# Kernel tuning notes

Hardware: AMD Instinct MI355X
Metric: run time of the kernel (lower is better)

The kernel has to match this reference:

```python
import jax, jax.numpy as jnp
import numpy as np

B, N, E = 8, 1024, 256
IN_DIMS, D_MODEL, H = 2, 64, 4
DH = D_MODEL // H  # 16


def _linear_params(key, fan_in, fan_out):
    k1, k2 = jax.random.split(key)
    bound = 1.0 / np.sqrt(fan_in)
    W = jax.random.uniform(k1, (fan_in, fan_out), jnp.float32, -bound, bound)
    b = jax.random.uniform(k2, (fan_out,), jnp.float32, -bound, bound)
    return W, b


def setup_inputs() -> dict:
    key = jax.random.key(0)
    ks = jax.random.split(key, 12)
    x = jax.random.normal(ks[0], (B, N, IN_DIMS), jnp.float32)
    edge_inital = jax.random.normal(ks[1], (B, H, E, DH), jnp.float32)
    C_edge_inital = jax.random.normal(ks[2], (B, H, E, DH), jnp.float32)
    G = jax.random.uniform(ks[3], (B, E, N), jnp.float32)
    C_G = jax.random.uniform(ks[4], (B, E, N), jnp.float32)
    W_emb, b_emb = _linear_params(ks[5], IN_DIMS, D_MODEL)
    W_q, b_q = _linear_params(ks[6], D_MODEL, D_MODEL)
    W_k, b_k = _linear_params(ks[7], D_MODEL, D_MODEL)
    W_eq, b_eq = _linear_params(ks[8], DH, DH)
    W_ek, b_ek = _linear_params(ks[9], DH, DH)
    W_ceq, b_ceq = _linear_params(ks[10], DH, DH)
    W_cek, b_cek = _linear_params(ks[11], DH, DH)
    return dict(x=x, edge_inital=edge_inital, C_edge_inital=C_edge_inital, G=G, C_G=C_G,
                W_emb=W_emb, b_emb=b_emb, W_q=W_q, b_q=b_q, W_k=W_k, b_k=b_k,
                W_eq=W_eq, b_eq=b_eq, W_ek=W_ek, b_ek=b_ek,
                W_ceq=W_ceq, b_ceq=b_ceq, W_cek=W_cek, b_cek=b_cek)


def _split_heads(t):
    # [B, N, D_MODEL] -> [B, H, N, DH]
    b, n, _ = t.shape
    return t.reshape(b, n, H, DH).transpose(0, 2, 1, 3)


def _branch(q, k, edge, Gm, We_q, be_q, We_k, be_k, scale):
    eq = edge @ We_q + be_q          # [B,H,E,DH]
    ek = edge @ We_k + be_k
    div = Gm.sum(axis=1)[:, None, :, None]  # [B,1,N,1]
    gq = q + jnp.einsum('ben,bhec->bhnc', Gm, eq) / div
    gk = k + jnp.einsum('ben,bhec->bhnc', Gm, ek) / div
    scores = jnp.einsum('bhnc,bhmc->bhnm', gq, gk) / scale
    return jax.nn.softmax(scores, axis=-1)


def reference(x, edge_inital, C_edge_inital, G, C_G,
              W_emb, b_emb, W_q, b_q, W_k, b_k,
              W_eq, b_eq, W_ek, b_ek, W_ceq, b_ceq, W_cek, b_cek):
    scale = jnp.sqrt(jnp.float32(D_MODEL))
    emb = x @ W_emb + b_emb                 # [B,N,D]
    q = _split_heads(emb @ W_q + b_q)       # [B,H,N,DH]
    k = _split_heads(emb @ W_k + b_k)
    g_att = _branch(q, k, edge_inital, G, W_eq, b_eq, W_ek, b_ek, scale)
    cg_att = _branch(q, k, C_edge_inital, C_G, W_ceq, b_ceq, W_cek, b_cek, scale)
    return (g_att, cg_att)
```

## Files before the change

### kernel.cpp

```cpp
#include <hip/hip_runtime.h>
#include <math.h>

#define BB     8
#define NN     1024
#define EE     256
#define DMODEL 64
#define HH     4
#define DHH    16

#define WS_Q    0
#define WS_K    524288
#define WS_EQ   1048576
#define WS_GQ   1572864
#define WS_GKT  2621440

__global__ __launch_bounds__(256) void qk_kernel(
    const float* __restrict__ x, const float* __restrict__ W_emb,
    const float* __restrict__ b_emb, const float* __restrict__ W_q,
    const float* __restrict__ b_q, const float* __restrict__ W_k,
    const float* __restrict__ b_k, float* __restrict__ ws) {
  __shared__ float semb[4][DMODEL];
  const int tid = threadIdx.x;
  const int p = tid >> 6, d = tid & 63;
  const int pos = blockIdx.x * 4 + p;
  const float x0 = x[pos * 2 + 0];
  const float x1 = x[pos * 2 + 1];
  semb[p][d] = fmaf(x0, W_emb[d], fmaf(x1, W_emb[DMODEL + d], b_emb[d]));
  __syncthreads();
  float accq = b_q[d], acck = b_k[d];
#pragma unroll 8
  for (int e = 0; e < DMODEL; ++e) {
    const float ev = semb[p][e];
    accq = fmaf(ev, W_q[e * DMODEL + d], accq);
    acck = fmaf(ev, W_k[e * DMODEL + d], acck);
  }
  const int b = pos >> 10, n = pos & (NN - 1);
  const int h = d >> 4, c = d & 15;
  const int oidx = ((b * HH + h) * NN + n) * DHH + c;
  ws[WS_Q + oidx] = accq;
  ws[WS_K + oidx] = acck;
}

__global__ __launch_bounds__(256) void edge_proj_kernel(
    const float* __restrict__ edge, const float* __restrict__ C_edge,
    const float* __restrict__ W_eq, const float* __restrict__ b_eq,
    const float* __restrict__ W_ek, const float* __restrict__ b_ek,
    const float* __restrict__ W_ceq, const float* __restrict__ b_ceq,
    const float* __restrict__ W_cek, const float* __restrict__ b_cek,
    float* __restrict__ ws) {
  const int t = blockIdx.x >> 5;
  const int row = ((blockIdx.x & 31) << 8) + threadIdx.x;
  const float* __restrict__ src = (t < 2) ? edge : C_edge;
  const float* __restrict__ W =
      (t == 0) ? W_eq : (t == 1) ? W_ek : (t == 2) ? W_ceq : W_cek;
  const float* __restrict__ bias =
      (t == 0) ? b_eq : (t == 1) ? b_ek : (t == 2) ? b_ceq : b_cek;
  float in[16];
  const float4* s4 = (const float4*)(src + row * 16);
#pragma unroll
  for (int i = 0; i < 4; ++i) {
    const float4 v = s4[i];
    in[4 * i + 0] = v.x; in[4 * i + 1] = v.y;
    in[4 * i + 2] = v.z; in[4 * i + 3] = v.w;
  }
  float outv[16];
#pragma unroll
  for (int c = 0; c < 16; ++c) outv[c] = bias[c];
#pragma unroll
  for (int cp = 0; cp < 16; ++cp) {
    const float iv = in[cp];
#pragma unroll
    for (int c = 0; c < 16; ++c) outv[c] = fmaf(iv, W[cp * 16 + c], outv[c]);
  }
  float4* o4 = (float4*)(ws + WS_EQ + t * 131072 + row * 16);
#pragma unroll
  for (int i = 0; i < 4; ++i)
    o4[i] = make_float4(outv[4 * i + 0], outv[4 * i + 1], outv[4 * i + 2],
                        outv[4 * i + 3]);
}

__global__ __launch_bounds__(256) void gqgk_kernel(
    const float* __restrict__ G, const float* __restrict__ C_G,
    float* __restrict__ ws) {
  const int sub = blockIdx.x & 7;
  const int mat = blockIdx.x >> 3;
  const int h = mat & 3;
  const int b = (mat >> 2) & 7;
  const int br = mat >> 5;
  const int nchunk = sub >> 1;
  const int c0 = (sub & 1) * 8;
  const int n = (nchunk << 8) + threadIdx.x;
  const float* __restrict__ Gm = br ? C_G : G;
  const float* __restrict__ eqp =
      ws + WS_EQ + (br * 2 + 0) * 131072 + (b * HH + h) * EE * 16 + c0;
  const float* __restrict__ ekp =
      ws + WS_EQ + (br * 2 + 1) * 131072 + (b * HH + h) * EE * 16 + c0;
  const float* __restrict__ gcol = Gm + b * EE * NN + n;
  float accq[8] = {0.f, 0.f, 0.f, 0.f, 0.f, 0.f, 0.f, 0.f};
  float acck[8] = {0.f, 0.f, 0.f, 0.f, 0.f, 0.f, 0.f, 0.f};
  float div = 0.f;
#pragma unroll 4
  for (int e = 0; e < EE; ++e) {
    const float g = gcol[e * NN];
    div += g;
#pragma unroll
    for (int c = 0; c < 8; ++c) {
      accq[c] = fmaf(g, eqp[e * 16 + c], accq[c]);
      acck[c] = fmaf(g, ekp[e * 16 + c], acck[c]);
    }
  }
  const float inv = 1.0f / div;
  const int qidx = ((b * HH + h) * NN + n) * 16 + c0;
  const float* __restrict__ qrow = ws + WS_Q + qidx;
  const float* __restrict__ krow = ws + WS_K + qidx;
  float* __restrict__ gq = ws + WS_GQ + (mat * NN + n) * 16 + c0;
  float* __restrict__ gkT = ws + WS_GKT + mat * 16 * NN + n;
#pragma unroll
  for (int c = 0; c < 8; ++c) {
    gq[c] = qrow[c] + accq[c] * inv;
    gkT[(c0 + c) * NN] = krow[c] + acck[c] * inv;
  }
}

__global__ __launch_bounds__(256, 2) void attn_kernel(
    const float* __restrict__ ws, float* __restrict__ out) {
  __shared__ float skT[16 * NN];
  const int idx = blockIdx.x;
  const int rb = idx & 31;
  const int mat = idx >> 5;
  const float* __restrict__ gkTp = ws + WS_GKT + mat * 16 * NN;
  const float* __restrict__ gqp = ws + WS_GQ + (mat * NN + rb * 32) * 16;
  const int tid = threadIdx.x;
  const float4* __restrict__ src4 = (const float4*)gkTp;
  float4* dst4 = (float4*)skT;
#pragma unroll
  for (int i = 0; i < 16; ++i) dst4[tid + 256 * i] = src4[tid + 256 * i];
  __syncthreads();
  const int wave = tid >> 6, lane = tid & 63;
  const int r0 = wave * 8;
  float s[8][16];
#pragma unroll
  for (int r = 0; r < 8; ++r)
#pragma unroll
    for (int t = 0; t < 16; ++t) s[r][t] = 0.f;

  for (int c = 0; c < 16; ++c) {
    float gkv[16];
#pragma unroll
    for (int t = 0; t < 16; ++t) gkv[t] = skT[c * NN + lane + 64 * t];
#pragma unroll
    for (int r = 0; r < 8; ++r) {
      const float qv = gqp[(r0 + r) * 16 + c];
#pragma unroll
      for (int t = 0; t < 16; ++t) s[r][t] = fmaf(qv, gkv[t], s[r][t]);
    }
  }

#pragma unroll
  for (int r = 0; r < 8; ++r) {
    float m = s[r][0];
#pragma unroll
    for (int t = 1; t < 16; ++t) m = fmaxf(m, s[r][t]);
#pragma unroll
    for (int off = 32; off; off >>= 1) m = fmaxf(m, __shfl_xor(m, off));
    float sum = 0.f;
#pragma unroll
    for (int t = 0; t < 16; ++t) {
      s[r][t] = __expf((s[r][t] - m) * 0.125f);
      sum += s[r][t];
    }
#pragma unroll
    for (int off = 32; off; off >>= 1) sum += __shfl_xor(sum, off);
    const float inv = 1.0f / sum;
    float* __restrict__ orow =
        out + ((size_t)mat * NN + (size_t)(rb * 32 + r0 + r)) * NN;
#pragma unroll
    for (int t = 0; t < 16; ++t) orow[lane + 64 * t] = s[r][t] * inv;
  }
}

extern "C" void kernel_launch(void* const* d_in, const int* in_sizes, int n_in,
                              void* d_out, int out_size, void* d_ws,
                              size_t ws_size, hipStream_t stream) {
  const float* x      = (const float*)d_in[0];
  const float* edge   = (const float*)d_in[1];
  const float* C_edge = (const float*)d_in[2];
  const float* G      = (const float*)d_in[3];
  const float* C_G    = (const float*)d_in[4];
  const float* W_emb  = (const float*)d_in[5];
  const float* b_emb  = (const float*)d_in[6];
  const float* W_q    = (const float*)d_in[7];
  const float* b_q    = (const float*)d_in[8];
  const float* W_k    = (const float*)d_in[9];
  const float* b_k    = (const float*)d_in[10];
  const float* W_eq   = (const float*)d_in[11];
  const float* b_eq   = (const float*)d_in[12];
  const float* W_ek   = (const float*)d_in[13];
  const float* b_ek   = (const float*)d_in[14];
  const float* W_ceq  = (const float*)d_in[15];
  const float* b_ceq  = (const float*)d_in[16];
  const float* W_cek  = (const float*)d_in[17];
  const float* b_cek  = (const float*)d_in[18];
  float* ws = (float*)d_ws;
  float* out = (float*)d_out;

  hipLaunchKernelGGL(qk_kernel, dim3(BB * NN / 4), dim3(256), 0, stream, x,
                     W_emb, b_emb, W_q, b_q, W_k, b_k, ws);
  hipLaunchKernelGGL(edge_proj_kernel, dim3(128), dim3(256), 0, stream, edge,
                     C_edge, W_eq, b_eq, W_ek, b_ek, W_ceq, b_ceq, W_cek,
                     b_cek, ws);
  hipLaunchKernelGGL(gqgk_kernel, dim3(512), dim3(256), 0, stream, G, C_G, ws);
  hipLaunchKernelGGL(attn_kernel, dim3(2 * BB * HH * (NN / 32)), dim3(256), 0,
                     stream, ws, out);
}
```

Measured before the change: 389.7 us.

## Fuse edge projection into gqgk kernel and enlarge attention blocks

Fuses the edge projection into the G-aggregation kernel, which now computes projected edge features into shared memory per block, so one launch and a workspace round trip go away. The aggregation grid grows to 1024 blocks with 4 channels each for more parallelism. The attention kernel moves to 1024-thread blocks covering 64 rows, which loads the transposed K once per 64 rows instead of per 32 rows and stages Q in shared memory. The cost is redundant edge projection work across blocks, more G re-reads across channel splits, and lower occupancy from large blocks with 64KB of shared memory.

```diff
diff --git a/kernel.cpp b/kernel.cpp
--- a/kernel.cpp
+++ b/kernel.cpp
@@ -10,9 +10,8 @@
 
 #define WS_Q    0
 #define WS_K    524288
-#define WS_EQ   1048576
-#define WS_GQ   1572864
-#define WS_GKT  2621440
+#define WS_GQ   1048576
+#define WS_GKT  2097152
 
 __global__ __launch_bounds__(256) void qk_kernel(
     const float* __restrict__ x, const float* __restrict__ W_emb,
@@ -41,72 +40,71 @@
   ws[WS_K + oidx] = acck;
 }
 
-__global__ __launch_bounds__(256) void edge_proj_kernel(
+__global__ __launch_bounds__(256) void gqgk_kernel(
+    const float* __restrict__ G, const float* __restrict__ C_G,
     const float* __restrict__ edge, const float* __restrict__ C_edge,
     const float* __restrict__ W_eq, const float* __restrict__ b_eq,
     const float* __restrict__ W_ek, const float* __restrict__ b_ek,
     const float* __restrict__ W_ceq, const float* __restrict__ b_ceq,
     const float* __restrict__ W_cek, const float* __restrict__ b_cek,
     float* __restrict__ ws) {
-  const int t = blockIdx.x >> 5;
-  const int row = ((blockIdx.x & 31) << 8) + threadIdx.x;
-  const float* __restrict__ src = (t < 2) ? edge : C_edge;
-  const float* __restrict__ W =
-      (t == 0) ? W_eq : (t == 1) ? W_ek : (t == 2) ? W_ceq : W_cek;
-  const float* __restrict__ bias =
-      (t == 0) ? b_eq : (t == 1) ? b_ek : (t == 2) ? b_ceq : b_cek;
-  float in[16];
-  const float4* s4 = (const float4*)(src + row * 16);
-#pragma unroll
-  for (int i = 0; i < 4; ++i) {
-    const float4 v = s4[i];
-    in[4 * i + 0] = v.x; in[4 * i + 1] = v.y;
-    in[4 * i + 2] = v.z; in[4 * i + 3] = v.w;
-  }
-  float outv[16];
-#pragma unroll
-  for (int c = 0; c < 16; ++c) outv[c] = bias[c];
-#pragma unroll
-  for (int cp = 0; cp < 16; ++cp) {
-    const float iv = in[cp];
-#pragma unroll
-    for (int c = 0; c < 16; ++c) outv[c] = fmaf(iv, W[cp * 16 + c], outv[c]);
-  }
-  float4* o4 = (float4*)(ws + WS_EQ + t * 131072 + row * 16);
-#pragma unroll
-  for (int i = 0; i < 4; ++i)
-    o4[i] = make_float4(outv[4 * i + 0], outv[4 * i + 1], outv[4 * i + 2],
-                        outv[4 * i + 3]);
-}
-
-__global__ __launch_bounds__(256) void gqgk_kernel(
-    const float* __restrict__ G, const float* __restrict__ C_G,
-    float* __restrict__ ws) {
-  const int sub = blockIdx.x & 7;
-  const int mat = blockIdx.x >> 3;
+  __shared__ float seq[EE * 4];
+  __shared__ float sek[EE * 4];
+  const int sub = blockIdx.x & 15;
+  const int mat = blockIdx.x >> 4;
   const int h = mat & 3;
   const int b = (mat >> 2) & 7;
   const int br = mat >> 5;
-  const int nchunk = sub >> 1;
-  const int c0 = (sub & 1) * 8;
-  const int n = (nchunk << 8) + threadIdx.x;
+  const int nchunk = sub >> 2;
+  const int c0 = (sub & 3) * 4;
+  const int tid = threadIdx.x;
+  const int n = (nchunk << 8) + tid;
+
+  const float* __restrict__ Wq = br ? W_ceq : W_eq;
+  const float* __restrict__ Wk = br ? W_cek : W_ek;
+  const float* __restrict__ bq = br ? b_ceq : b_eq;
+  const float* __restrict__ bk = br ? b_cek : b_ek;
+  const float* __restrict__ esrc = br ? C_edge : edge;
+
+  {
+    float in[16];
+    const float4* s4 = (const float4*)(esrc + ((size_t)(b * HH + h) * EE + tid) * 16);
+#pragma unroll
+    for (int i = 0; i < 4; ++i) {
+      const float4 v = s4[i];
+      in[4 * i + 0] = v.x; in[4 * i + 1] = v.y;
+      in[4 * i + 2] = v.z; in[4 * i + 3] = v.w;
+    }
+    float aq[4], ak[4];
+#pragma unroll
+    for (int j = 0; j < 4; ++j) { aq[j] = bq[c0 + j]; ak[j] = bk[c0 + j]; }
+#pragma unroll
+    for (int cp = 0; cp < 16; ++cp) {
+      const float iv = in[cp];
+#pragma unroll
+      for (int j = 0; j < 4; ++j) {
+        aq[j] = fmaf(iv, Wq[cp * 16 + c0 + j], aq[j]);
+        ak[j] = fmaf(iv, Wk[cp * 16 + c0 + j], ak[j]);
+      }
+    }
+#pragma unroll
+    for (int j = 0; j < 4; ++j) { seq[tid * 4 + j] = aq[j]; sek[tid * 4 + j] = ak[j]; }
+  }
+  __syncthreads();
+
   const float* __restrict__ Gm = br ? C_G : G;
-  const float* __restrict__ eqp =
-      ws + WS_EQ + (br * 2 + 0) * 131072 + (b * HH + h) * EE * 16 + c0;
-  const float* __restrict__ ekp =
-      ws + WS_EQ + (br * 2 + 1) * 131072 + (b * HH + h) * EE * 16 + c0;
-  const float* __restrict__ gcol = Gm + b * EE * NN + n;
-  float accq[8] = {0.f, 0.f, 0.f, 0.f, 0.f, 0.f, 0.f, 0.f};
-  float acck[8] = {0.f, 0.f, 0.f, 0.f, 0.f, 0.f, 0.f, 0.f};
+  const float* __restrict__ gcol = Gm + (size_t)b * EE * NN + n;
+  float accq[4] = {0.f, 0.f, 0.f, 0.f};
+  float acck[4] = {0.f, 0.f, 0.f, 0.f};
   float div = 0.f;
-#pragma unroll 4
+#pragma unroll 8
   for (int e = 0; e < EE; ++e) {
     const float g = gcol[e * NN];
     div += g;
 #pragma unroll
-    for (int c = 0; c < 8; ++c) {
-      accq[c] = fmaf(g, eqp[e * 16 + c], accq[c]);
-      acck[c] = fmaf(g, ekp[e * 16 + c], acck[c]);
+    for (int c = 0; c < 4; ++c) {
+      accq[c] = fmaf(g, seq[e * 4 + c], accq[c]);
+      acck[c] = fmaf(g, sek[e * 4 + c], acck[c]);
     }
   }
   const float inv = 1.0f / div;
@@ -115,32 +113,38 @@
   const float* __restrict__ krow = ws + WS_K + qidx;
   float* __restrict__ gq = ws + WS_GQ + (mat * NN + n) * 16 + c0;
   float* __restrict__ gkT = ws + WS_GKT + mat * 16 * NN + n;
-#pragma unroll
-  for (int c = 0; c < 8; ++c) {
-    gq[c] = qrow[c] + accq[c] * inv;
+  float4 qo;
+  qo.x = qrow[0] + accq[0] * inv;
+  qo.y = qrow[1] + accq[1] * inv;
+  qo.z = qrow[2] + accq[2] * inv;
+  qo.w = qrow[3] + accq[3] * inv;
+  *(float4*)gq = qo;
+#pragma unroll
+  for (int c = 0; c < 4; ++c)
     gkT[(c0 + c) * NN] = krow[c] + acck[c] * inv;
-  }
-}
-
-__global__ __launch_bounds__(256, 2) void attn_kernel(
+}
+
+__global__ __launch_bounds__(1024) void attn_kernel(
     const float* __restrict__ ws, float* __restrict__ out) {
   __shared__ float skT[16 * NN];
+  __shared__ float sgq[64 * 16];
   const int idx = blockIdx.x;
-  const int rb = idx & 31;
-  const int mat = idx >> 5;
+  const int rb = idx & 15;
+  const int mat = idx >> 4;
   const float* __restrict__ gkTp = ws + WS_GKT + mat * 16 * NN;
-  const float* __restrict__ gqp = ws + WS_GQ + (mat * NN + rb * 32) * 16;
+  const float* __restrict__ gqp = ws + WS_GQ + (mat * NN + rb * 64) * 16;
   const int tid = threadIdx.x;
   const float4* __restrict__ src4 = (const float4*)gkTp;
   float4* dst4 = (float4*)skT;
 #pragma unroll
-  for (int i = 0; i < 16; ++i) dst4[tid + 256 * i] = src4[tid + 256 * i];
+  for (int i = 0; i < 4; ++i) dst4[tid + 1024 * i] = src4[tid + 1024 * i];
+  if (tid < 256) ((float4*)sgq)[tid] = ((const float4*)gqp)[tid];
   __syncthreads();
   const int wave = tid >> 6, lane = tid & 63;
-  const int r0 = wave * 8;
-  float s[8][16];
-#pragma unroll
-  for (int r = 0; r < 8; ++r)
+  const int r0 = wave * 4;
+  float s[4][16];
+#pragma unroll
+  for (int r = 0; r < 4; ++r)
 #pragma unroll
     for (int t = 0; t < 16; ++t) s[r][t] = 0.f;
 
@@ -149,15 +153,15 @@
 #pragma unroll
     for (int t = 0; t < 16; ++t) gkv[t] = skT[c * NN + lane + 64 * t];
 #pragma unroll
-    for (int r = 0; r < 8; ++r) {
-      const float qv = gqp[(r0 + r) * 16 + c];
+    for (int r = 0; r < 4; ++r) {
+      const float qv = sgq[(r0 + r) * 16 + c];
 #pragma unroll
       for (int t = 0; t < 16; ++t) s[r][t] = fmaf(qv, gkv[t], s[r][t]);
     }
   }
 
 #pragma unroll
-  for (int r = 0; r < 8; ++r) {
+  for (int r = 0; r < 4; ++r) {
     float m = s[r][0];
 #pragma unroll
     for (int t = 1; t < 16; ++t) m = fmaxf(m, s[r][t]);
@@ -173,7 +177,7 @@
     for (int off = 32; off; off >>= 1) sum += __shfl_xor(sum, off);
     const float inv = 1.0f / sum;
     float* __restrict__ orow =
-        out + ((size_t)mat * NN + (size_t)(rb * 32 + r0 + r)) * NN;
+        out + ((size_t)mat * NN + (size_t)(rb * 64 + r0 + r)) * NN;
 #pragma unroll
     for (int t = 0; t < 16; ++t) orow[lane + 64 * t] = s[r][t] * inv;
   }
@@ -206,10 +210,9 @@
 
   hipLaunchKernelGGL(qk_kernel, dim3(BB * NN / 4), dim3(256), 0, stream, x,
                      W_emb, b_emb, W_q, b_q, W_k, b_k, ws);
-  hipLaunchKernelGGL(edge_proj_kernel, dim3(128), dim3(256), 0, stream, edge,
-                     C_edge, W_eq, b_eq, W_ek, b_ek, W_ceq, b_ceq, W_cek,
-                     b_cek, ws);
-  hipLaunchKernelGGL(gqgk_kernel, dim3(512), dim3(256), 0, stream, G, C_G, ws);
-  hipLaunchKernelGGL(attn_kernel, dim3(2 * BB * HH * (NN / 32)), dim3(256), 0,
+  hipLaunchKernelGGL(gqgk_kernel, dim3(2 * BB * HH * 16), dim3(256), 0, stream,
+                     G, C_G, edge, C_edge, W_eq, b_eq, W_ek, b_ek, W_ceq,
+                     b_ceq, W_cek, b_cek, ws);
+  hipLaunchKernelGGL(attn_kernel, dim3(2 * BB * HH * 16), dim3(1024), 0,
                      stream, ws, out);
 }
```

New measurement: 381.2 us. -2.2%, faster.
